# Kernel tuning notes

Hardware: AMD Instinct MI355X
Metric: run time of the kernel (lower is better)

The kernel has to match this reference:

```python
import jax, jax.numpy as jnp
import numpy as np

B, S, D, H = 2, 2048, 1024, 16
DH = D // H  # head dim = 64


def setup_inputs() -> dict:
    key = jax.random.key(0)
    ks = jax.random.split(key, 8)
    q = jax.random.normal(ks[0], (B, S, D), dtype=jnp.float32)
    k = jax.random.normal(ks[1], (B, S, D), dtype=jnp.float32)
    v = jax.random.normal(ks[2], (B, S, D), dtype=jnp.float32)
    attn_mask = jax.random.randint(ks[3], (1, 1, S, S), 0, 2, dtype=jnp.int32)
    sc = 1.0 / np.sqrt(D)
    Wq = (jax.random.normal(ks[4], (D, D), dtype=jnp.float32) * sc)
    Wk = (jax.random.normal(ks[5], (D, D), dtype=jnp.float32) * sc)
    Wv = (jax.random.normal(ks[6], (D, D), dtype=jnp.float32) * sc)
    Wo = (jax.random.normal(ks[7], (D, D), dtype=jnp.float32) * sc)
    return {"q": q, "k": k, "v": v, "attn_mask": attn_mask,
            "Wq": Wq, "Wk": Wk, "Wv": Wv, "Wo": Wo}


def reference(q, k, v, attn_mask, Wq, Wk, Wv, Wo):
    bs = q.shape[0]
    # torch Linear: y = x @ W.T ; split heads -> [B, H, S, DH]
    qh = (q @ Wq.T).reshape(bs, -1, H, DH).transpose(0, 2, 1, 3)
    kh = (k @ Wk.T).reshape(bs, -1, H, DH).transpose(0, 2, 1, 3)
    vh = (v @ Wv.T).reshape(bs, -1, H, DH).transpose(0, 2, 1, 3)
    # scaled dot-product attention with explicit [B,H,S,S] scores
    scores = jnp.einsum('bhqd,bhkd->bhqk', qh, kh) / jnp.sqrt(
        jnp.asarray(DH, dtype=qh.dtype))
    scores = jnp.where(attn_mask == 0, jnp.asarray(-1e34, scores.dtype), scores)
    attn = jax.nn.softmax(scores, axis=-1)
    out = jnp.einsum('bhqk,bhkd->bhqd', attn, vh)
    out = out.transpose(0, 2, 1, 3).reshape(bs, -1, H * DH)
    out = out @ Wo.T
    return (out, attn)
```

## Files before the change

kernel.cpp:

```cpp
#include <hip/hip_runtime.h>
#include <stdint.h>

#define S_ 2048
#define NKT_ 32
#define LP 72

typedef short bf16x8 __attribute__((ext_vector_type(8)));
typedef float f32x4 __attribute__((ext_vector_type(4)));

__device__ __forceinline__ short f2bf(float x) {
  union { float f; uint32_t u; } v; v.f = x;
  uint32_t r = v.u + 0x7fffu + ((v.u >> 16) & 1u);
  return (short)(r >> 16);
}
__device__ __forceinline__ float bf2f(short s) {
  union { uint32_t u; float f; } v; v.u = ((uint32_t)(uint16_t)s) << 16;
  return v.f;
}

__device__ __forceinline__ bf16x8 ld8(const void* base, long off, int isf32) {
  bf16x8 r;
  if (isf32) {
    const float* p = (const float*)base + off;
    f32x4 a = *(const f32x4*)p;
    f32x4 b = *(const f32x4*)(p + 4);
    r[0] = f2bf(a[0]); r[1] = f2bf(a[1]); r[2] = f2bf(a[2]); r[3] = f2bf(a[3]);
    r[4] = f2bf(b[0]); r[5] = f2bf(b[1]); r[6] = f2bf(b[2]); r[7] = f2bf(b[3]);
  } else {
    r = *(const bf16x8*)((const short*)base + off);
  }
  return r;
}

__global__ __launch_bounds__(256) void detect_dtype(const uint32_t* __restrict__ q,
                                                    uint32_t* __restrict__ flag) {
  __shared__ int cnt;
  int t = threadIdx.x;
  if (t == 0) cnt = 0;
  __syncthreads();
  uint32_t w = q[t];
  int e = (int)((w >> 7) & 0xFF);
  int hit = (e >= 100 && e <= 141) ? 1 : 0;
  atomicAdd(&cnt, hit);
  __syncthreads();
  if (t == 0) *flag = (cnt >= 200) ? 0u : 1u;
}

template <int MODE>
__device__ __forceinline__ void gemm_body(short* sA, short* sW,
    const void* A, const void* W, int fA, int fW,
    short* __restrict__ dst, float* __restrict__ dstF, int outf) {
  const int tid = threadIdx.x;
  const int wave = tid >> 6, lane = tid & 63;
  const int quad = lane >> 4, l16 = lane & 15;
  const int m0 = blockIdx.x * 128, n0 = blockIdx.y * 128;
  const int wm = wave >> 1, wn = wave & 1;

  f32x4 acc[4][4] = {};

  for (int k0 = 0; k0 < 1024; k0 += 64) {
    for (int c = tid; c < 1024; c += 256) {
      int r = c >> 3, ch = c & 7;
      *(bf16x8*)(sA + r * LP + ch * 8) = ld8(A, (long)(m0 + r) * 1024 + k0 + ch * 8, fA);
      *(bf16x8*)(sW + r * LP + ch * 8) = ld8(W, (long)(n0 + r) * 1024 + k0 + ch * 8, fW);
    }
    __syncthreads();
    const short* Pa = (MODE == 2) ? sW : sA;
    const short* Pb = (MODE == 2) ? sA : sW;
#pragma unroll
    for (int kk = 0; kk < 2; ++kk) {
      bf16x8 af[4], bfr[4];
#pragma unroll
      for (int i = 0; i < 4; ++i)
        af[i] = *(const bf16x8*)(Pa + (wm * 64 + i * 16 + l16) * LP + (kk * 4 + quad) * 8);
#pragma unroll
      for (int j = 0; j < 4; ++j)
        bfr[j] = *(const bf16x8*)(Pb + (wn * 64 + j * 16 + l16) * LP + (kk * 4 + quad) * 8);
#pragma unroll
      for (int i = 0; i < 4; ++i)
#pragma unroll
        for (int j = 0; j < 4; ++j)
          acc[i][j] = __builtin_amdgcn_mfma_f32_16x16x32_bf16(af[i], bfr[j], acc[i][j], 0, 0, 0);
    }
    __syncthreads();
  }

#pragma unroll
  for (int i = 0; i < 4; ++i)
#pragma unroll
    for (int j = 0; j < 4; ++j)
#pragma unroll
      for (int r = 0; r < 4; ++r) {
        float vv = acc[i][j][r];
        if (MODE == 0) vv *= 0.18033688011112042f;
        if (MODE == 2) {
          int n = n0 + wm * 64 + i * 16 + quad * 4 + r;
          int m = m0 + wn * 64 + j * 16 + l16;
          int b = m >> 11, s = m & 2047, h = n >> 6, dh = n & 63;
          dst[((long)((b * 16 + h) * 64 + dh)) * 2048 + s] = f2bf(vv);
        } else {
          int m = m0 + wm * 64 + i * 16 + quad * 4 + r;
          int n = n0 + wn * 64 + j * 16 + l16;
          if (MODE == 3) {
            if (outf) dstF[(long)m * 1024 + n] = vv;
            else      dst[(long)m * 1024 + n] = f2bf(vv);
          } else {
            int b = m >> 11, s = m & 2047, h = n >> 6, dh = n & 63;
            dst[((long)(b * 16 + h) * 2048 + s) * 64 + dh] = f2bf(vv);
          }
        }
      }
}

__global__ __launch_bounds__(256) void qkv_kernel(
    const void* __restrict__ q, const void* __restrict__ k, const void* __restrict__ v,
    const void* __restrict__ Wq, const void* __restrict__ Wk, const void* __restrict__ Wv,
    const uint32_t* __restrict__ flag,
    short* __restrict__ qh, short* __restrict__ kh, short* __restrict__ vt) {
  __shared__ __align__(16) short sA[128 * LP];
  __shared__ __align__(16) short sW[128 * LP];
  const int f = (int)*flag;
  if (blockIdx.z == 0)      gemm_body<0>(sA, sW, q, Wq, f, f, qh, nullptr, 0);
  else if (blockIdx.z == 1) gemm_body<1>(sA, sW, k, Wk, f, f, kh, nullptr, 0);
  else                      gemm_body<2>(sA, sW, v, Wv, f, f, vt, nullptr, 0);
}

__global__ __launch_bounds__(256) void oproj_kernel(
    const short* __restrict__ o, const void* __restrict__ Wo,
    const uint32_t* __restrict__ flag,
    short* __restrict__ outB, float* __restrict__ outF) {
  __shared__ __align__(16) short sA[128 * LP];
  __shared__ __align__(16) short sW[128 * LP];
  const int f = (int)*flag;
  gemm_body<3>(sA, sW, (const void*)o, Wo, 0, f, outB, outF, f);
}

__global__ __launch_bounds__(256) void pack_mask(const int* __restrict__ mask,
                                                 uint32_t* __restrict__ bits) {
  int gt = blockIdx.x * 256 + threadIdx.x;
  int wid = gt >> 6, lane = gt & 63;
  int nw = (gridDim.x * 256) >> 6;
  for (int g = wid; g < (S_ * S_) / 64; g += nw) {
    int v = mask[(long)g * 64 + lane];
    unsigned long long b = __ballot(v != 0);
    if (lane == 0) bits[2 * g] = (uint32_t)b;
    if (lane == 1) bits[2 * g + 1] = (uint32_t)(b >> 32);
  }
}

__global__ __launch_bounds__(256) void attn_kernel(
    const short* __restrict__ qh, const short* __restrict__ kh,
    const short* __restrict__ vt, const uint32_t* __restrict__ mbits,
    const uint32_t* __restrict__ flag,
    short* __restrict__ attnB, float* __restrict__ attnF, short* __restrict__ o) {
  __shared__ __align__(16) short sK[64 * LP];
  __shared__ __align__(16) short sV[64 * LP];
  __shared__ __align__(16) short sP[4][32 * LP];
  const int tid = threadIdx.x;
  const int wave = tid >> 6, lane = tid & 63;
  const int quad = lane >> 4, l16 = lane & 15;
  const int q0 = blockIdx.x * 128;
  const int bh = blockIdx.y;
  const int outf = (int)*flag;
  const short* Qb = qh + (long)bh * S_ * 64;
  const short* Kb = kh + (long)bh * S_ * 64;
  const short* Vb = vt + (long)bh * 64 * S_;
  short* attnBb = attnB + (long)bh * S_ * S_;
  float* attnFb = attnF + (long)bh * S_ * S_;
  short* sPw = sP[wave];
  const uint32_t cm0 = 1u << l16, cm1 = 1u << (l16 + 16);

  bf16x8 qf[2][2];
#pragma unroll
  for (int i = 0; i < 2; ++i)
#pragma unroll
    for (int kk = 0; kk < 2; ++kk)
      qf[i][kk] = *(const bf16x8*)(Qb + (long)(q0 + wave * 32 + i * 16 + l16) * 64 + kk * 32 + quad * 8);

  float mrun[2][4], lrun[2][4];
#pragma unroll
  for (int i = 0; i < 2; ++i)
#pragma unroll
    for (int r = 0; r < 4; ++r) { mrun[i][r] = -3e38f; lrun[i][r] = 0.f; }

  for (int kt = 0; kt < NKT_; ++kt) {
    const int k0 = kt * 64;
    for (int c = tid; c < 512; c += 256) {
      int r = c >> 3, ch = c & 7;
      *(bf16x8*)(sK + r * LP + ch * 8) = *(const bf16x8*)(Kb + (long)(k0 + r) * 64 + ch * 8);
    }
    __syncthreads();
    f32x4 acc[2][4] = {};
#pragma unroll
    for (int kk = 0; kk < 2; ++kk) {
      bf16x8 bfr[4];
#pragma unroll
      for (int j = 0; j < 4; ++j)
        bfr[j] = *(const bf16x8*)(sK + (j * 16 + l16) * LP + (kk * 4 + quad) * 8);
#pragma unroll
      for (int i = 0; i < 2; ++i)
#pragma unroll
        for (int j = 0; j < 4; ++j)
          acc[i][j] = __builtin_amdgcn_mfma_f32_16x16x32_bf16(qf[i][kk], bfr[j], acc[i][j], 0, 0, 0);
    }
#pragma unroll
    for (int i = 0; i < 2; ++i)
#pragma unroll
      for (int r = 0; r < 4; ++r) {
        int qrow = q0 + wave * 32 + i * 16 + quad * 4 + r;
        const uint32_t* wp = mbits + qrow * 64 + (k0 >> 5);
        uint32_t w0 = wp[0], w1 = wp[1];
        float s0 = (w0 & cm0) ? acc[i][0][r] : -1e30f;
        float s1 = (w0 & cm1) ? acc[i][1][r] : -1e30f;
        float s2 = (w1 & cm0) ? acc[i][2][r] : -1e30f;
        float s3 = (w1 & cm1) ? acc[i][3][r] : -1e30f;
        float mx = fmaxf(fmaxf(s0, s1), fmaxf(s2, s3));
        mx = fmaxf(mx, __shfl_xor(mx, 1));
        mx = fmaxf(mx, __shfl_xor(mx, 2));
        mx = fmaxf(mx, __shfl_xor(mx, 4));
        mx = fmaxf(mx, __shfl_xor(mx, 8));
        float mold = mrun[i][r];
        float mnew = fmaxf(mold, mx);
        float sum = exp2f(s0 - mnew) + exp2f(s1 - mnew) + exp2f(s2 - mnew) + exp2f(s3 - mnew);
        sum += __shfl_xor(sum, 1);
        sum += __shfl_xor(sum, 2);
        sum += __shfl_xor(sum, 4);
        sum += __shfl_xor(sum, 8);
        lrun[i][r] = lrun[i][r] * exp2f(mold - mnew) + sum;
        mrun[i][r] = mnew;
      }
    __syncthreads();
  }

  float invl[2][4];
#pragma unroll
  for (int i = 0; i < 2; ++i)
#pragma unroll
    for (int r = 0; r < 4; ++r) invl[i][r] = 1.0f / lrun[i][r];

  f32x4 acco[2][4] = {};

  for (int kt = 0; kt < NKT_; ++kt) {
    const int k0 = kt * 64;
    for (int c = tid; c < 512; c += 256) {
      int r = c >> 3, ch = c & 7;
      *(bf16x8*)(sK + r * LP + ch * 8) = *(const bf16x8*)(Kb + (long)(k0 + r) * 64 + ch * 8);
      *(bf16x8*)(sV + r * LP + ch * 8) = *(const bf16x8*)(Vb + (long)r * S_ + k0 + ch * 8);
    }
    __syncthreads();
    f32x4 acc[2][4] = {};
#pragma unroll
    for (int kk = 0; kk < 2; ++kk) {
      bf16x8 bfr[4];
#pragma unroll
      for (int j = 0; j < 4; ++j)
        bfr[j] = *(const bf16x8*)(sK + (j * 16 + l16) * LP + (kk * 4 + quad) * 8);
#pragma unroll
      for (int i = 0; i < 2; ++i)
#pragma unroll
        for (int j = 0; j < 4; ++j)
          acc[i][j] = __builtin_amdgcn_mfma_f32_16x16x32_bf16(qf[i][kk], bfr[j], acc[i][j], 0, 0, 0);
    }
#pragma unroll
    for (int i = 0; i < 2; ++i)
#pragma unroll
      for (int r = 0; r < 4; ++r) {
        int qrow = q0 + wave * 32 + i * 16 + quad * 4 + r;
        const uint32_t* wp = mbits + qrow * 64 + (k0 >> 5);
        uint32_t w0 = wp[0], w1 = wp[1];
        float mm = mrun[i][r], il = invl[i][r];
        float s0 = (w0 & cm0) ? acc[i][0][r] : -1e30f;
        float s1 = (w0 & cm1) ? acc[i][1][r] : -1e30f;
        float s2 = (w1 & cm0) ? acc[i][2][r] : -1e30f;
        float s3 = (w1 & cm1) ? acc[i][3][r] : -1e30f;
        int rowL = i * 16 + quad * 4 + r;
        short* rp = sPw + rowL * LP;
        rp[0  + l16] = f2bf(exp2f(s0 - mm) * il);
        rp[16 + l16] = f2bf(exp2f(s1 - mm) * il);
        rp[32 + l16] = f2bf(exp2f(s2 - mm) * il);
        rp[48 + l16] = f2bf(exp2f(s3 - mm) * il);
      }
    __syncthreads();
    bf16x8 vf[2][4];
#pragma unroll
    for (int kk = 0; kk < 2; ++kk)
#pragma unroll
      for (int jd = 0; jd < 4; ++jd)
        vf[kk][jd] = *(const bf16x8*)(sV + (jd * 16 + l16) * LP + (kk * 4 + quad) * 8);
#pragma unroll
    for (int kk = 0; kk < 2; ++kk)
#pragma unroll
      for (int i = 0; i < 2; ++i) {
        bf16x8 pf = *(const bf16x8*)(sPw + (i * 16 + l16) * LP + (kk * 4 + quad) * 8);
#pragma unroll
        for (int jd = 0; jd < 4; ++jd)
          acco[i][jd] = __builtin_amdgcn_mfma_f32_16x16x32_bf16(pf, vf[kk][jd], acco[i][jd], 0, 0, 0);
      }
#pragma unroll
    for (int it = 0; it < 4; ++it) {
      int cid = it * 64 + lane;
      int rowL = cid >> 3, kc = cid & 7;
      bf16x8 vals = *(const bf16x8*)(sPw + rowL * LP + kc * 8);
      long base = (long)(q0 + wave * 32 + rowL) * S_ + k0 + kc * 8;
      if (outf) {
        f32x4 lo, hi;
#pragma unroll
        for (int e = 0; e < 4; ++e) { lo[e] = bf2f(vals[e]); hi[e] = bf2f(vals[e + 4]); }
        *(f32x4*)(attnFb + base) = lo;
        *(f32x4*)(attnFb + base + 4) = hi;
      } else {
        *(bf16x8*)(attnBb + base) = vals;
      }
    }
    __syncthreads();
  }

  const int b = bh >> 4, h = bh & 15;
#pragma unroll
  for (int i = 0; i < 2; ++i)
#pragma unroll
    for (int jd = 0; jd < 4; ++jd)
#pragma unroll
      for (int r = 0; r < 4; ++r) {
        int qrow = q0 + wave * 32 + i * 16 + quad * 4 + r;
        int dh = jd * 16 + l16;
        o[(long)(b * S_ + qrow) * 1024 + h * 64 + dh] = f2bf(acco[i][jd][r]);
      }
}

extern "C" void kernel_launch(void* const* d_in, const int* in_sizes, int n_in,
                              void* d_out, int out_size, void* d_ws, size_t ws_size,
                              hipStream_t stream) {
  (void)in_sizes; (void)n_in; (void)out_size; (void)ws_size;
  const void* q  = d_in[0];
  const void* k  = d_in[1];
  const void* v  = d_in[2];
  const int* mask = (const int*)d_in[3];
  const void* Wq = d_in[4];
  const void* Wk = d_in[5];
  const void* Wv = d_in[6];
  const void* Wo = d_in[7];

  short* outB  = (short*)d_out;
  short* attnB = outB + (long)4194304;
  float* outF  = (float*)d_out;
  float* attnF = outF + (long)4194304;

  short* qh = (short*)d_ws;
  short* kh = qh + (long)4194304;
  short* vt = kh + (long)4194304;
  short* o  = vt + (long)4194304;
  uint32_t* mbits = (uint32_t*)(o + (long)4194304);
  uint32_t* flag  = mbits + 131072;

  detect_dtype<<<dim3(1), dim3(256), 0, stream>>>((const uint32_t*)q, flag);
  pack_mask<<<dim3(256), dim3(256), 0, stream>>>(mask, mbits);
  qkv_kernel<<<dim3(32, 8, 3), dim3(256), 0, stream>>>(q, k, v, Wq, Wk, Wv, flag, qh, kh, vt);
  attn_kernel<<<dim3(16, 32), dim3(256), 0, stream>>>(qh, kh, vt, mbits, flag, attnB, attnF, o);
  oproj_kernel<<<dim3(32, 8), dim3(256), 0, stream>>>(o, Wo, flag, outB, outF);
}
```

Measured before the change: 997.4 us.

## Pre-convert inputs to bf16, use direct global-to-LDS loads with XOR swizzle, double-buffer attention K/V

After: 889.9 us. 10.8% less time.

```diff
diff --git a/kernel.cpp b/kernel.cpp
--- a/kernel.cpp
+++ b/kernel.cpp
@@ -18,18 +18,9 @@
   return v.f;
 }
 
-__device__ __forceinline__ bf16x8 ld8(const void* base, long off, int isf32) {
-  bf16x8 r;
-  if (isf32) {
-    const float* p = (const float*)base + off;
-    f32x4 a = *(const f32x4*)p;
-    f32x4 b = *(const f32x4*)(p + 4);
-    r[0] = f2bf(a[0]); r[1] = f2bf(a[1]); r[2] = f2bf(a[2]); r[3] = f2bf(a[3]);
-    r[4] = f2bf(b[0]); r[5] = f2bf(b[1]); r[6] = f2bf(b[2]); r[7] = f2bf(b[3]);
-  } else {
-    r = *(const bf16x8*)((const short*)base + off);
-  }
-  return r;
+__device__ __forceinline__ void gload16(const void* g, void* l) {
+  __builtin_amdgcn_global_load_lds((const __attribute__((address_space(1))) void*)g,
+                                   (__attribute__((address_space(3))) void*)l, 16, 0, 0);
 }
 
 __global__ __launch_bounds__(256) void detect_dtype(const uint32_t* __restrict__ q,
@@ -46,9 +37,50 @@
   if (t == 0) *flag = (cnt >= 200) ? 0u : 1u;
 }
 
+__device__ __forceinline__ void cvt_body(const void* __restrict__ src,
+                                         short* __restrict__ d, long n8, int f) {
+  long i = (long)blockIdx.x * 256 + threadIdx.x;
+  const long stride = (long)gridDim.x * 256;
+  if (f) {
+    const f32x4* s = (const f32x4*)src;
+    for (; i < n8; i += stride) {
+      f32x4 a = s[2 * i], b = s[2 * i + 1];
+      bf16x8 r;
+      r[0] = f2bf(a[0]); r[1] = f2bf(a[1]); r[2] = f2bf(a[2]); r[3] = f2bf(a[3]);
+      r[4] = f2bf(b[0]); r[5] = f2bf(b[1]); r[6] = f2bf(b[2]); r[7] = f2bf(b[3]);
+      *(bf16x8*)(d + i * 8) = r;
+    }
+  } else {
+    const bf16x8* s = (const bf16x8*)src;
+    for (; i < n8; i += stride) *(bf16x8*)(d + i * 8) = s[i];
+  }
+}
+
+__global__ __launch_bounds__(256) void to_bf16_batch(
+    const void* __restrict__ q, const void* __restrict__ k, const void* __restrict__ v,
+    const void* __restrict__ wq, const void* __restrict__ wk, const void* __restrict__ wv,
+    short* __restrict__ dst, const uint32_t* __restrict__ flag) {
+  const void* src; long n8; long doff;
+  switch (blockIdx.y) {
+    case 0:  src = q;  n8 = 524288; doff = 0;        break;
+    case 1:  src = k;  n8 = 524288; doff = 4194304;  break;
+    case 2:  src = v;  n8 = 524288; doff = 8388608;  break;
+    case 3:  src = wq; n8 = 131072; doff = 12582912; break;
+    case 4:  src = wk; n8 = 131072; doff = 13631488; break;
+    default: src = wv; n8 = 131072; doff = 14680064; break;
+  }
+  cvt_body(src, dst + doff, n8, (int)*flag);
+}
+
+__global__ __launch_bounds__(256) void to_bf16_one(const void* __restrict__ src,
+                                                   short* __restrict__ dst, long n8,
+                                                   const uint32_t* __restrict__ flag) {
+  cvt_body(src, dst, n8, (int)*flag);
+}
+
 template <int MODE>
 __device__ __forceinline__ void gemm_body(short* sA, short* sW,
-    const void* A, const void* W, int fA, int fW,
+    const short* __restrict__ A, const short* __restrict__ W,
     short* __restrict__ dst, float* __restrict__ dstF, int outf) {
   const int tid = threadIdx.x;
   const int wave = tid >> 6, lane = tid & 63;
@@ -59,23 +91,27 @@
   f32x4 acc[4][4] = {};
 
   for (int k0 = 0; k0 < 1024; k0 += 64) {
-    for (int c = tid; c < 1024; c += 256) {
-      int r = c >> 3, ch = c & 7;
-      *(bf16x8*)(sA + r * LP + ch * 8) = ld8(A, (long)(m0 + r) * 1024 + k0 + ch * 8, fA);
-      *(bf16x8*)(sW + r * LP + ch * 8) = ld8(W, (long)(n0 + r) * 1024 + k0 + ch * 8, fW);
+#pragma unroll
+    for (int it = 0; it < 4; ++it) {
+      int c = it * 256 + tid;
+      int r = c >> 3, cs = (c & 7) ^ (r & 7);
+      int ldsoff = (it * 256 + wave * 64) * 8;
+      gload16(A + (long)(m0 + r) * 1024 + k0 + cs * 8, sA + ldsoff);
+      gload16(W + (long)(n0 + r) * 1024 + k0 + cs * 8, sW + ldsoff);
     }
     __syncthreads();
     const short* Pa = (MODE == 2) ? sW : sA;
     const short* Pb = (MODE == 2) ? sA : sW;
 #pragma unroll
     for (int kk = 0; kk < 2; ++kk) {
+      const int cx = ((kk * 4 + quad) ^ (l16 & 7)) * 8;
       bf16x8 af[4], bfr[4];
 #pragma unroll
       for (int i = 0; i < 4; ++i)
-        af[i] = *(const bf16x8*)(Pa + (wm * 64 + i * 16 + l16) * LP + (kk * 4 + quad) * 8);
+        af[i] = *(const bf16x8*)(Pa + (wm * 64 + i * 16 + l16) * 64 + cx);
 #pragma unroll
       for (int j = 0; j < 4; ++j)
-        bfr[j] = *(const bf16x8*)(Pb + (wn * 64 + j * 16 + l16) * LP + (kk * 4 + quad) * 8);
+        bfr[j] = *(const bf16x8*)(Pb + (wn * 64 + j * 16 + l16) * 64 + cx);
 #pragma unroll
       for (int i = 0; i < 4; ++i)
 #pragma unroll
@@ -113,26 +149,23 @@
 }
 
 __global__ __launch_bounds__(256) void qkv_kernel(
-    const void* __restrict__ q, const void* __restrict__ k, const void* __restrict__ v,
-    const void* __restrict__ Wq, const void* __restrict__ Wk, const void* __restrict__ Wv,
-    const uint32_t* __restrict__ flag,
+    const short* __restrict__ qb, const short* __restrict__ kb, const short* __restrict__ vb,
+    const short* __restrict__ Wqb, const short* __restrict__ Wkb, const short* __restrict__ Wvb,
     short* __restrict__ qh, short* __restrict__ kh, short* __restrict__ vt) {
-  __shared__ __align__(16) short sA[128 * LP];
-  __shared__ __align__(16) short sW[128 * LP];
-  const int f = (int)*flag;
-  if (blockIdx.z == 0)      gemm_body<0>(sA, sW, q, Wq, f, f, qh, nullptr, 0);
-  else if (blockIdx.z == 1) gemm_body<1>(sA, sW, k, Wk, f, f, kh, nullptr, 0);
-  else                      gemm_body<2>(sA, sW, v, Wv, f, f, vt, nullptr, 0);
+  __shared__ __align__(16) short sA[128 * 64];
+  __shared__ __align__(16) short sW[128 * 64];
+  if (blockIdx.z == 0)      gemm_body<0>(sA, sW, qb, Wqb, qh, nullptr, 0);
+  else if (blockIdx.z == 1) gemm_body<1>(sA, sW, kb, Wkb, kh, nullptr, 0);
+  else                      gemm_body<2>(sA, sW, vb, Wvb, vt, nullptr, 0);
 }
 
 __global__ __launch_bounds__(256) void oproj_kernel(
-    const short* __restrict__ o, const void* __restrict__ Wo,
+    const short* __restrict__ o, const short* __restrict__ Wob,
     const uint32_t* __restrict__ flag,
     short* __restrict__ outB, float* __restrict__ outF) {
-  __shared__ __align__(16) short sA[128 * LP];
-  __shared__ __align__(16) short sW[128 * LP];
-  const int f = (int)*flag;
-  gemm_body<3>(sA, sW, (const void*)o, Wo, 0, f, outB, outF, f);
+  __shared__ __align__(16) short sA[128 * 64];
+  __shared__ __align__(16) short sW[128 * 64];
+  gemm_body<3>(sA, sW, o, Wob, outB, outF, (int)*flag);
 }
 
 __global__ __launch_bounds__(256) void pack_mask(const int* __restrict__ mask,
@@ -153,8 +186,8 @@
     const short* __restrict__ vt, const uint32_t* __restrict__ mbits,
     const uint32_t* __restrict__ flag,
     short* __restrict__ attnB, float* __restrict__ attnF, short* __restrict__ o) {
-  __shared__ __align__(16) short sK[64 * LP];
-  __shared__ __align__(16) short sV[64 * LP];
+  __shared__ __align__(16) short sK[2][64 * 64];
+  __shared__ __align__(16) short sV[2][64 * 64];
   __shared__ __align__(16) short sP[4][32 * LP];
   const int tid = threadIdx.x;
   const int wave = tid >> 6, lane = tid & 63;
@@ -170,6 +203,23 @@
   short* sPw = sP[wave];
   const uint32_t cm0 = 1u << l16, cm1 = 1u << (l16 + 16);
 
+  auto stageK = [&](int kt, int b) {
+#pragma unroll
+    for (int it = 0; it < 2; ++it) {
+      int c = it * 256 + tid;
+      int r = c >> 3, cs = (c & 7) ^ (r & 7);
+      gload16(Kb + (long)(kt * 64 + r) * 64 + cs * 8, &sK[b][(it * 256 + wave * 64) * 8]);
+    }
+  };
+  auto stageV = [&](int kt, int b) {
+#pragma unroll
+    for (int it = 0; it < 2; ++it) {
+      int c = it * 256 + tid;
+      int r = c >> 3, cs = (c & 7) ^ (r & 7);
+      gload16(Vb + (long)r * S_ + kt * 64 + cs * 8, &sV[b][(it * 256 + wave * 64) * 8]);
+    }
+  };
+
   bf16x8 qf[2][2];
 #pragma unroll
   for (int i = 0; i < 2; ++i)
@@ -183,20 +233,20 @@
 #pragma unroll
     for (int r = 0; r < 4; ++r) { mrun[i][r] = -3e38f; lrun[i][r] = 0.f; }
 
+  stageK(0, 0);
+  __syncthreads();
+  int buf = 0;
   for (int kt = 0; kt < NKT_; ++kt) {
     const int k0 = kt * 64;
-    for (int c = tid; c < 512; c += 256) {
-      int r = c >> 3, ch = c & 7;
-      *(bf16x8*)(sK + r * LP + ch * 8) = *(const bf16x8*)(Kb + (long)(k0 + r) * 64 + ch * 8);
-    }
-    __syncthreads();
+    if (kt + 1 < NKT_) stageK(kt + 1, buf ^ 1);
     f32x4 acc[2][4] = {};
 #pragma unroll
     for (int kk = 0; kk < 2; ++kk) {
+      const int cx = ((kk * 4 + quad) ^ (l16 & 7)) * 8;
       bf16x8 bfr[4];
 #pragma unroll
       for (int j = 0; j < 4; ++j)
-        bfr[j] = *(const bf16x8*)(sK + (j * 16 + l16) * LP + (kk * 4 + quad) * 8);
+        bfr[j] = *(const bf16x8*)(&sK[buf][(j * 16 + l16) * 64 + cx]);
 #pragma unroll
       for (int i = 0; i < 2; ++i)
 #pragma unroll
@@ -230,6 +280,7 @@
         mrun[i][r] = mnew;
       }
     __syncthreads();
+    buf ^= 1;
   }
 
   float invl[2][4];
@@ -240,21 +291,20 @@
 
   f32x4 acco[2][4] = {};
 
+  stageK(0, 0); stageV(0, 0);
+  __syncthreads();
+  buf = 0;
   for (int kt = 0; kt < NKT_; ++kt) {
     const int k0 = kt * 64;
-    for (int c = tid; c < 512; c += 256) {
-      int r = c >> 3, ch = c & 7;
-      *(bf16x8*)(sK + r * LP + ch * 8) = *(const bf16x8*)(Kb + (long)(k0 + r) * 64 + ch * 8);
-      *(bf16x8*)(sV + r * LP + ch * 8) = *(const bf16x8*)(Vb + (long)r * S_ + k0 + ch * 8);
-    }
-    __syncthreads();
+    if (kt + 1 < NKT_) { stageK(kt + 1, buf ^ 1); stageV(kt + 1, buf ^ 1); }
     f32x4 acc[2][4] = {};
 #pragma unroll
     for (int kk = 0; kk < 2; ++kk) {
+      const int cx = ((kk * 4 + quad) ^ (l16 & 7)) * 8;
       bf16x8 bfr[4];
 #pragma unroll
       for (int j = 0; j < 4; ++j)
-        bfr[j] = *(const bf16x8*)(sK + (j * 16 + l16) * LP + (kk * 4 + quad) * 8);
+        bfr[j] = *(const bf16x8*)(&sK[buf][(j * 16 + l16) * 64 + cx]);
 #pragma unroll
       for (int i = 0; i < 2; ++i)
 #pragma unroll
@@ -280,22 +330,8 @@
         rp[32 + l16] = f2bf(exp2f(s2 - mm) * il);
         rp[48 + l16] = f2bf(exp2f(s3 - mm) * il);
       }
-    __syncthreads();
-    bf16x8 vf[2][4];
-#pragma unroll
-    for (int kk = 0; kk < 2; ++kk)
-#pragma unroll
-      for (int jd = 0; jd < 4; ++jd)
-        vf[kk][jd] = *(const bf16x8*)(sV + (jd * 16 + l16) * LP + (kk * 4 + quad) * 8);
-#pragma unroll
-    for (int kk = 0; kk < 2; ++kk)
-#pragma unroll
-      for (int i = 0; i < 2; ++i) {
-        bf16x8 pf = *(const bf16x8*)(sPw + (i * 16 + l16) * LP + (kk * 4 + quad) * 8);
-#pragma unroll
-        for (int jd = 0; jd < 4; ++jd)
-          acco[i][jd] = __builtin_amdgcn_mfma_f32_16x16x32_bf16(pf, vf[kk][jd], acco[i][jd], 0, 0, 0);
-      }
+    asm volatile("s_waitcnt lgkmcnt(0)" ::: "memory");
+    __builtin_amdgcn_sched_barrier(0);
 #pragma unroll
     for (int it = 0; it < 4; ++it) {
       int cid = it * 64 + lane;
@@ -312,7 +348,25 @@
         *(bf16x8*)(attnBb + base) = vals;
       }
     }
+    bf16x8 vf[2][4];
+#pragma unroll
+    for (int kk = 0; kk < 2; ++kk) {
+      const int cx = ((kk * 4 + quad) ^ (l16 & 7)) * 8;
+#pragma unroll
+      for (int jd = 0; jd < 4; ++jd)
+        vf[kk][jd] = *(const bf16x8*)(&sV[buf][(jd * 16 + l16) * 64 + cx]);
+    }
+#pragma unroll
+    for (int kk = 0; kk < 2; ++kk)
+#pragma unroll
+      for (int i = 0; i < 2; ++i) {
+        bf16x8 pf = *(const bf16x8*)(sPw + (i * 16 + l16) * LP + (kk * 4 + quad) * 8);
+#pragma unroll
+        for (int jd = 0; jd < 4; ++jd)
+          acco[i][jd] = __builtin_amdgcn_mfma_f32_16x16x32_bf16(pf, vf[kk][jd], acco[i][jd], 0, 0, 0);
+      }
     __syncthreads();
+    buf ^= 1;
   }
 
   const int b = bh >> 4, h = bh & 15;
@@ -353,9 +407,19 @@
   uint32_t* mbits = (uint32_t*)(o + (long)4194304);
   uint32_t* flag  = mbits + 131072;
 
+  short* qb  = (short*)((char*)d_out + (20l << 20));
+  short* kb  = qb  + (long)4194304;
+  short* vb  = kb  + (long)4194304;
+  short* wqb = vb  + (long)4194304;
+  short* wkb = wqb + (long)1048576;
+  short* wvb = wkb + (long)1048576;
+  short* wob = qh;
+
   detect_dtype<<<dim3(1), dim3(256), 0, stream>>>((const uint32_t*)q, flag);
   pack_mask<<<dim3(256), dim3(256), 0, stream>>>(mask, mbits);
-  qkv_kernel<<<dim3(32, 8, 3), dim3(256), 0, stream>>>(q, k, v, Wq, Wk, Wv, flag, qh, kh, vt);
+  to_bf16_batch<<<dim3(512, 6), dim3(256), 0, stream>>>(q, k, v, Wq, Wk, Wv, qb, flag);
+  qkv_kernel<<<dim3(32, 8, 3), dim3(256), 0, stream>>>(qb, kb, vb, wqb, wkb, wvb, qh, kh, vt);
   attn_kernel<<<dim3(16, 32), dim3(256), 0, stream>>>(qh, kh, vt, mbits, flag, attnB, attnF, o);
-  oproj_kernel<<<dim3(32, 8), dim3(256), 0, stream>>>(o, Wo, flag, outB, outF);
-}
+  to_bf16_one<<<dim3(512), dim3(256), 0, stream>>>(Wo, wob, 131072, flag);
+  oproj_kernel<<<dim3(32, 8), dim3(256), 0, stream>>>(o, wob, flag, outB, outF);
+}
```
